# Optimization experiments

Hardware: AMD Instinct MI355X
Metric: run time of the kernel (lower is better)

The kernel has to match this reference:

```python
import jax, jax.numpy as jnp
import numpy as np

N = 100000
D = 128
H = 128
E = 1600000


def setup_inputs() -> dict:
    key = jax.random.key(0)
    ks = jax.random.split(key, 9)
    x = jax.random.normal(ks[0], (N, D), dtype=jnp.float32)
    edge_index = jax.random.randint(ks[1], (2, E), 0, N, dtype=jnp.int64)
    s = 1.0 / np.sqrt(D)
    W1 = jax.random.uniform(ks[2], (D, H), jnp.float32, -s, s)
    b1 = jnp.zeros((H,), jnp.float32)
    s2 = 1.0 / np.sqrt(H)
    W2 = jax.random.uniform(ks[3], (H, H), jnp.float32, -s2, s2)
    b2 = jnp.zeros((H,), jnp.float32)
    Wo = jax.random.uniform(ks[4], (H, 1), jnp.float32, -s2, s2)
    bo = jax.random.uniform(ks[5], (1,), jnp.float32, -s2, s2)
    return {"x": x, "edge_index": edge_index, "W1": W1, "b1": b1,
            "W2": W2, "b2": b2, "Wo": Wo, "bo": bo}


def _gcn_layer(x, W, b, src, dst, dinv):
    # PyG GCNConv: h = x @ W; out = D^-1/2 (A+I) D^-1/2 h + b
    h = x @ W                                   # [N, H]
    norm = dinv[src] * dinv[dst]                # [E]
    msg = h[src] * norm[:, None]                # [E, H] gathered messages
    agg = jax.ops.segment_sum(msg, dst, num_segments=N)
    agg = agg + h * (dinv * dinv)[:, None]      # self-loop contribution
    return agg + b


def reference(x, edge_index, W1, b1, W2, b2, Wo, bo):
    src, dst = edge_index[0], edge_index[1]
    # degree with self-loops, counted on destination (col), edge_weight = 1
    deg = jax.ops.segment_sum(jnp.ones((E,), jnp.float32), dst, num_segments=N) + 1.0
    dinv = deg ** -0.5                          # [N]
    h = jax.nn.relu(_gcn_layer(x, W1, b1, src, dst, dinv))
    h = _gcn_layer(h, W2, b2, src, dst, dinv)
    out = h @ Wo + bo                            # [N, 1]
    return out[:, 0]                             # [N]
```

## Files before the change

### kernel.cpp

```cpp
#include <hip/hip_runtime.h>
#include <hip/hip_fp16.h>

#define DIM 128
#define NPB 256
#define BCAP 5120
#define T_SCAT 4096

typedef _Float16 half8 __attribute__((ext_vector_type(8)));
typedef float floatx4 __attribute__((ext_vector_type(4)));
typedef float floatx2 __attribute__((ext_vector_type(2)));

__device__ __forceinline__ void gemm_block(const float* __restrict__ X,
                                           const __half* __restrict__ w1frag,
                                           unsigned char* __restrict__ A,
                                           int N, int gb) {
    const int t = threadIdx.x;
    const int w = t >> 6, l = t & 63;
    const int q = l >> 4;
    const int node = gb * 64 + w * 16 + (l & 15);
    const bool valid = node < N;
    half8 bfrag[4];
#pragma unroll
    for (int ks = 0; ks < 4; ks++) {
        float4 f0 = make_float4(0, 0, 0, 0), f1 = make_float4(0, 0, 0, 0);
        if (valid) {
            const float* px = X + (size_t)node * DIM + ks * 32 + q * 8;
            f0 = *(const float4*)px;
            f1 = *(const float4*)(px + 4);
        }
        bfrag[ks][0] = (_Float16)f0.x; bfrag[ks][1] = (_Float16)f0.y;
        bfrag[ks][2] = (_Float16)f0.z; bfrag[ks][3] = (_Float16)f0.w;
        bfrag[ks][4] = (_Float16)f1.x; bfrag[ks][5] = (_Float16)f1.y;
        bfrag[ks][6] = (_Float16)f1.z; bfrag[ks][7] = (_Float16)f1.w;
    }
    const half8* wf = (const half8*)w1frag;
#pragma unroll
    for (int ct = 0; ct < 8; ct++) {
        floatx4 acc = {0.f, 0.f, 0.f, 0.f};
#pragma unroll
        for (int ks = 0; ks < 4; ks++) {
            half8 afrag = wf[(ct * 4 + ks) * 64 + l];
            acc = __builtin_amdgcn_mfma_f32_16x16x32_f16(afrag, bfrag[ks], acc, 0, 0, 0);
        }
        if (valid) {
            int st = 0;
            st = __builtin_amdgcn_cvt_pk_fp8_f32(acc[0], acc[1], st, false);
            st = __builtin_amdgcn_cvt_pk_fp8_f32(acc[2], acc[3], st, true);
            *(int*)(A + (size_t)node * DIM + ct * 16 + q * 4) = st;
        }
    }
}

__global__ void prep_k(const float* __restrict__ W1, const float* __restrict__ W2,
                       const float* __restrict__ Wo, const float* __restrict__ b2,
                       const float* __restrict__ bo,
                       __half* __restrict__ w1frag, float* __restrict__ w2o,
                       float* __restrict__ cbuf, int* __restrict__ bcur) {
    if (blockIdx.x < 8) {
        int idx = blockIdx.x * 256 + threadIdx.x;
        int ct = idx >> 8, ks = (idx >> 6) & 3, l = idx & 63;
        int m = l & 15, q = l >> 4;
        half8 vals;
#pragma unroll
        for (int j = 0; j < 8; j++)
            vals[j] = (_Float16)W1[(ks * 32 + q * 8 + j) * DIM + ct * 16 + m];
        ((half8*)w1frag)[idx] = vals;
    } else if (blockIdx.x == 8) {
        int t = threadIdx.x;
        if (t < 128) {
            float s = 0.f;
            for (int k = 0; k < 128; k++) s += W2[t * 128 + k] * Wo[k];
            w2o[t] = s;
        }
        if (t == 0) {
            float c = bo[0];
            for (int k = 0; k < 128; k++) c += b2[k] * Wo[k];
            cbuf[0] = c;
        }
    } else {
#pragma unroll
        for (int i = 0; i < 4; i++) bcur[threadIdx.x + i * 256] = 0;
    }
}

__global__ __launch_bounds__(256) void scatter_gemm_k(
        const int* __restrict__ ei, int E, int ntiles,
        int2* __restrict__ be, int* __restrict__ bcur,
        const float* __restrict__ X, const __half* __restrict__ w1frag,
        unsigned char* __restrict__ A, int N) {
    if (blockIdx.x >= (unsigned)ntiles) {
        gemm_block(X, w1frag, A, N, blockIdx.x - ntiles);
        return;
    }
    __shared__ int lcnt[1024];
    __shared__ int lscan[1024];
    __shared__ int lbase[1024];
    __shared__ int wsum[4];
    __shared__ int2 stage[T_SCAT];
    const int t = threadIdx.x;
    const int lane = t & 63, w = t >> 6;
    const int tile0 = blockIdx.x * T_SCAT;
    int tcnt = E - tile0; if (tcnt > T_SCAT) tcnt = T_SCAT;
    for (int i = t; i < 1024; i += 256) lcnt[i] = 0;
    __syncthreads();
    for (int i = t; i < tcnt; i += 256)
        atomicAdd(&lcnt[ei[E + tile0 + i] >> 8], 1);
    __syncthreads();
    const int b4 = t * 4;
    int c0 = lcnt[b4], c1 = lcnt[b4 + 1], c2 = lcnt[b4 + 2], c3 = lcnt[b4 + 3];
    int s4 = c0 + c1 + c2 + c3;
    int v = s4;
#pragma unroll
    for (int off = 1; off < 64; off <<= 1) {
        int u = __shfl_up(v, off, 64);
        if (lane >= off) v += u;
    }
    if (lane == 63) wsum[w] = v;
    __syncthreads();
    int wbase = 0;
#pragma unroll
    for (int i = 0; i < 4; i++) wbase += (i < w) ? wsum[i] : 0;
    int run = wbase + v - s4;
    lscan[b4] = run;
    if (c0) lbase[b4] = b4 * BCAP + atomicAdd(&bcur[b4], c0);
    run += c0; lscan[b4 + 1] = run;
    if (c1) lbase[b4 + 1] = (b4 + 1) * BCAP + atomicAdd(&bcur[b4 + 1], c1);
    run += c1; lscan[b4 + 2] = run;
    if (c2) lbase[b4 + 2] = (b4 + 2) * BCAP + atomicAdd(&bcur[b4 + 2], c2);
    run += c2; lscan[b4 + 3] = run;
    if (c3) lbase[b4 + 3] = (b4 + 3) * BCAP + atomicAdd(&bcur[b4 + 3], c3);
    lcnt[b4] = 0; lcnt[b4 + 1] = 0; lcnt[b4 + 2] = 0; lcnt[b4 + 3] = 0;
    __syncthreads();
    for (int i = t; i < tcnt; i += 256) {
        int s = ei[tile0 + i];
        int d = ei[E + tile0 + i];
        int b = d >> 8;
        int r = atomicAdd(&lcnt[b], 1);
        stage[lscan[b] + r] = make_int2(s, d);
    }
    __syncthreads();
    for (int i = t; i < tcnt; i += 256) {
        int2 ed = stage[i];
        int b = ed.y >> 8;
        be[lbase[b] + (i - lscan[b])] = ed;
    }
}

__global__ __launch_bounds__(256) void sort_gemm_k(
        const int2* __restrict__ be, const int* __restrict__ bcur,
        int* __restrict__ csr, int* __restrict__ rp, int* __restrict__ re,
        float* __restrict__ dinv, int N, int nb,
        const float* __restrict__ X, const __half* __restrict__ w1frag,
        unsigned char* __restrict__ A, int gemmBase) {
    if (blockIdx.x >= (unsigned)nb) {
        gemm_block(X, w1frag, A, N, gemmBase + blockIdx.x - nb);
        return;
    }
    __shared__ int lcnt[256];
    __shared__ int lscan[256];
    __shared__ int lc2[256];
    __shared__ int wsum[4];
    __shared__ int stage[BCAP];
    const int t = threadIdx.x;
    const int lane = t & 63, w = t >> 6;
    const int b = blockIdx.x;
    const int s = b * BCAP;
    int cnt = bcur[b]; if (cnt > BCAP) cnt = BCAP;
    lcnt[t] = 0; lc2[t] = 0;
    __syncthreads();
    for (int i = t; i < cnt; i += 256)
        atomicAdd(&lcnt[be[s + i].y & 255], 1);
    __syncthreads();
    int v = lcnt[t];
    int iv = v;
#pragma unroll
    for (int off = 1; off < 64; off <<= 1) {
        int u = __shfl_up(iv, off, 64);
        if (lane >= off) iv += u;
    }
    if (lane == 63) wsum[w] = iv;
    __syncthreads();
    int wbase = 0;
#pragma unroll
    for (int i = 0; i < 4; i++) wbase += (i < w) ? wsum[i] : 0;
    int excl = wbase + iv - v;
    lscan[t] = excl;
    int node = b * NPB + t;
    if (node < N) {
        rp[node] = s + excl;
        re[node] = s + excl + v;
        dinv[node] = rsqrtf((float)v + 1.0f);
    }
    __syncthreads();
    for (int i = t; i < cnt; i += 256) {
        int2 ed = be[s + i];
        int d = ed.y & 255;
        int r = atomicAdd(&lc2[d], 1);
        stage[lscan[d] + r] = ed.x;
    }
    __syncthreads();
    for (int i = t; i < cnt; i += 256) csr[s + i] = stage[i];
}

__device__ __forceinline__ void dec8(int2 r, float* f) {
    floatx2 a = __builtin_amdgcn_cvt_pk_f32_fp8(r.x, false);
    floatx2 b = __builtin_amdgcn_cvt_pk_f32_fp8(r.x, true);
    floatx2 c = __builtin_amdgcn_cvt_pk_f32_fp8(r.y, false);
    floatx2 d = __builtin_amdgcn_cvt_pk_f32_fp8(r.y, true);
    f[0] = a[0]; f[1] = a[1]; f[2] = b[0]; f[3] = b[1];
    f[4] = c[0]; f[5] = c[1]; f[6] = d[0]; f[7] = d[1];
}

__global__ __launch_bounds__(256) void agg1_k(const unsigned char* __restrict__ A,
                                              const int* __restrict__ rp,
                                              const int* __restrict__ re,
                                              const int* __restrict__ csr_src,
                                              const float* __restrict__ dinv,
                                              const float* __restrict__ b1,
                                              const float* __restrict__ w2o,
                                              float* __restrict__ z, int N) {
    const int li = threadIdx.x & 31;
    const int node = blockIdx.x * 8 + (threadIdx.x >> 5);
    if (node >= N) return;
    const int eoff = (li & 15) * 8;
    const float dn = dinv[node];
    const int s0 = rp[node], s1 = re[node];
    float acc[8];
    {
        int2 raw = *(const int2*)(A + (size_t)node * DIM + eoff);
        float hv[8]; dec8(raw, hv);
        float w0 = (li < 16) ? dn * dn : 0.f;
#pragma unroll
        for (int e = 0; e < 8; e++) acc[e] = hv[e] * w0;
    }
    for (int base = s0; base < s1; base += 32) {
        int sidx = 0; float dsl = 0.f;
        if (base + li < s1) { sidx = csr_src[base + li]; dsl = dinv[sidx]; }
        int nloc = s1 - base; if (nloc > 32) nloc = 32;
        int npair = (nloc + 1) >> 1;
#pragma unroll 2
        for (int j = 0; j < npair; j++) {
            int sel = 2 * j + (li >> 4);
            int ssrc = __shfl(sidx, sel, 32);
            float wgt = __shfl(dsl, sel, 32) * dn;
            int2 hraw = *(const int2*)(A + (size_t)ssrc * DIM + eoff);
            float h[8]; dec8(hraw, h);
#pragma unroll
            for (int e = 0; e < 8; e++) acc[e] = fmaf(h[e], wgt, acc[e]);
        }
    }
#pragma unroll
    for (int e = 0; e < 8; e++) acc[e] += __shfl_xor(acc[e], 16, 32);
    float sum = 0.f;
    if (li < 16) {
        float4 b0 = *(const float4*)(b1 + eoff);
        float4 b3 = *(const float4*)(b1 + eoff + 4);
        float4 w0 = *(const float4*)(w2o + eoff);
        float4 w3 = *(const float4*)(w2o + eoff + 4);
        sum  = fmaxf(acc[0] + b0.x, 0.f) * w0.x;
        sum += fmaxf(acc[1] + b0.y, 0.f) * w0.y;
        sum += fmaxf(acc[2] + b0.z, 0.f) * w0.z;
        sum += fmaxf(acc[3] + b0.w, 0.f) * w0.w;
        sum += fmaxf(acc[4] + b3.x, 0.f) * w3.x;
        sum += fmaxf(acc[5] + b3.y, 0.f) * w3.y;
        sum += fmaxf(acc[6] + b3.z, 0.f) * w3.z;
        sum += fmaxf(acc[7] + b3.w, 0.f) * w3.w;
    }
#pragma unroll
    for (int off = 16; off > 0; off >>= 1) sum += __shfl_down(sum, off, 32);
    if (li == 0) z[node] = sum;
}

__global__ void final_k(const float* __restrict__ z, const float* __restrict__ dinv,
                        const int* __restrict__ rp, const int* __restrict__ re,
                        const int* __restrict__ csr_src,
                        const float* __restrict__ cbuf, float* __restrict__ out, int N) {
    int n = blockIdx.x * 256 + threadIdx.x;
    if (n >= N) return;
    float dn = dinv[n];
    int s0 = rp[n], s1 = re[n];
    float s = 0.f;
    for (int i = s0; i < s1; i++) {
        int sx = csr_src[i];
        s = fmaf(dinv[sx], z[sx], s);
    }
    out[n] = fmaf(dn, s, fmaf(dn * dn, z[n], cbuf[0]));
}

extern "C" void kernel_launch(void* const* d_in, const int* in_sizes, int n_in,
                              void* d_out, int out_size, void* d_ws, size_t ws_size,
                              hipStream_t stream) {
    const float* x  = (const float*)d_in[0];
    const int*   ei = (const int*)d_in[1];
    const float* W1 = (const float*)d_in[2];
    const float* b1 = (const float*)d_in[3];
    const float* W2 = (const float*)d_in[4];
    const float* b2 = (const float*)d_in[5];
    const float* Wo = (const float*)d_in[6];
    const float* bo = (const float*)d_in[7];
    float* out = (float*)d_out;

    const int N = in_sizes[0] / DIM;
    const int E = in_sizes[1] / 2;
    const int NB = (N + NPB - 1) >> 8;
    const int ntiles = (E + T_SCAT - 1) / T_SCAT;
    const int ngemm = (N + 63) / 64;
    const int g1 = ngemm / 2;
    const int g2 = ngemm - g1;

    char* p = (char*)d_ws;
    auto alloc = [&](size_t bytes) {
        void* r = (void*)p;
        p += (bytes + 255) & ~size_t(255);
        return r;
    };
    unsigned char* A = (unsigned char*)alloc((size_t)N * DIM);
    int2*  be     = (int2*)alloc((size_t)NB * BCAP * 8);
    int*   csr    = (int*)alloc((size_t)NB * BCAP * 4);
    float* z      = (float*)alloc((size_t)N * 4);
    float* dinv   = (float*)alloc((size_t)N * 4);
    float* w2o    = (float*)alloc(128 * 4);
    float* cbuf   = (float*)alloc(16);
    __half* w1frag= (__half*)alloc(2048 * 8 * 2);
    int* rp       = (int*)alloc((size_t)N * 4);
    int* re       = (int*)alloc((size_t)N * 4);
    int* bcur     = (int*)alloc(1024 * 4);

    prep_k<<<10, 256, 0, stream>>>(W1, W2, Wo, b2, bo, w1frag, w2o, cbuf, bcur);
    scatter_gemm_k<<<ntiles + g1, 256, 0, stream>>>(ei, E, ntiles, be, bcur,
                                                    x, w1frag, A, N);
    sort_gemm_k<<<NB + g2, 256, 0, stream>>>(be, bcur, csr, rp, re, dinv, N, NB,
                                             x, w1frag, A, g1);
    agg1_k<<<(N + 7) / 8, 256, 0, stream>>>(A, rp, re, csr, dinv, b1, w2o, z, N);
    final_k<<<(N + 255) / 256, 256, 0, stream>>>(z, dinv, rp, re, csr, cbuf, out, N);
}
```

Baseline: 232.2 us.

## Fuse bucket sort with layer-1 aggregation and compute degrees via global atomics

```diff
diff --git a/kernel.cpp b/kernel.cpp
--- a/kernel.cpp
+++ b/kernel.cpp
@@ -85,7 +85,7 @@
 
 __global__ __launch_bounds__(256) void scatter_gemm_k(
         const int* __restrict__ ei, int E, int ntiles,
-        int2* __restrict__ be, int* __restrict__ bcur,
+        int2* __restrict__ be, int* __restrict__ bcur, int* __restrict__ deg,
         const float* __restrict__ X, const __half* __restrict__ w1frag,
         unsigned char* __restrict__ A, int N) {
     if (blockIdx.x >= (unsigned)ntiles) {
@@ -103,8 +103,11 @@
     int tcnt = E - tile0; if (tcnt > T_SCAT) tcnt = T_SCAT;
     for (int i = t; i < 1024; i += 256) lcnt[i] = 0;
     __syncthreads();
-    for (int i = t; i < tcnt; i += 256)
-        atomicAdd(&lcnt[ei[E + tile0 + i] >> 8], 1);
+    for (int i = t; i < tcnt; i += 256) {
+        int d = ei[E + tile0 + i];
+        atomicAdd(&lcnt[d >> 8], 1);
+        atomicAdd(&deg[d], 1);
+    }
     __syncthreads();
     const int b4 = t * 4;
     int c0 = lcnt[b4], c1 = lcnt[b4 + 1], c2 = lcnt[b4 + 2], c3 = lcnt[b4 + 3];
@@ -146,62 +149,6 @@
     }
 }
 
-__global__ __launch_bounds__(256) void sort_gemm_k(
-        const int2* __restrict__ be, const int* __restrict__ bcur,
-        int* __restrict__ csr, int* __restrict__ rp, int* __restrict__ re,
-        float* __restrict__ dinv, int N, int nb,
-        const float* __restrict__ X, const __half* __restrict__ w1frag,
-        unsigned char* __restrict__ A, int gemmBase) {
-    if (blockIdx.x >= (unsigned)nb) {
-        gemm_block(X, w1frag, A, N, gemmBase + blockIdx.x - nb);
-        return;
-    }
-    __shared__ int lcnt[256];
-    __shared__ int lscan[256];
-    __shared__ int lc2[256];
-    __shared__ int wsum[4];
-    __shared__ int stage[BCAP];
-    const int t = threadIdx.x;
-    const int lane = t & 63, w = t >> 6;
-    const int b = blockIdx.x;
-    const int s = b * BCAP;
-    int cnt = bcur[b]; if (cnt > BCAP) cnt = BCAP;
-    lcnt[t] = 0; lc2[t] = 0;
-    __syncthreads();
-    for (int i = t; i < cnt; i += 256)
-        atomicAdd(&lcnt[be[s + i].y & 255], 1);
-    __syncthreads();
-    int v = lcnt[t];
-    int iv = v;
-#pragma unroll
-    for (int off = 1; off < 64; off <<= 1) {
-        int u = __shfl_up(iv, off, 64);
-        if (lane >= off) iv += u;
-    }
-    if (lane == 63) wsum[w] = iv;
-    __syncthreads();
-    int wbase = 0;
-#pragma unroll
-    for (int i = 0; i < 4; i++) wbase += (i < w) ? wsum[i] : 0;
-    int excl = wbase + iv - v;
-    lscan[t] = excl;
-    int node = b * NPB + t;
-    if (node < N) {
-        rp[node] = s + excl;
-        re[node] = s + excl + v;
-        dinv[node] = rsqrtf((float)v + 1.0f);
-    }
-    __syncthreads();
-    for (int i = t; i < cnt; i += 256) {
-        int2 ed = be[s + i];
-        int d = ed.y & 255;
-        int r = atomicAdd(&lc2[d], 1);
-        stage[lscan[d] + r] = ed.x;
-    }
-    __syncthreads();
-    for (int i = t; i < cnt; i += 256) csr[s + i] = stage[i];
-}
-
 __device__ __forceinline__ void dec8(int2 r, float* f) {
     floatx2 a = __builtin_amdgcn_cvt_pk_f32_fp8(r.x, false);
     floatx2 b = __builtin_amdgcn_cvt_pk_f32_fp8(r.x, true);
@@ -211,64 +158,119 @@
     f[4] = c[0]; f[5] = c[1]; f[6] = d[0]; f[7] = d[1];
 }
 
-__global__ __launch_bounds__(256) void agg1_k(const unsigned char* __restrict__ A,
-                                              const int* __restrict__ rp,
-                                              const int* __restrict__ re,
-                                              const int* __restrict__ csr_src,
-                                              const float* __restrict__ dinv,
-                                              const float* __restrict__ b1,
-                                              const float* __restrict__ w2o,
-                                              float* __restrict__ z, int N) {
-    const int li = threadIdx.x & 31;
-    const int node = blockIdx.x * 8 + (threadIdx.x >> 5);
-    if (node >= N) return;
+__global__ __launch_bounds__(1024) void sort_agg_k(
+        const int2* __restrict__ be, const int* __restrict__ bcur,
+        const int* __restrict__ deg,
+        int* __restrict__ csr, int* __restrict__ rp, int* __restrict__ re,
+        float* __restrict__ dinv,
+        const unsigned char* __restrict__ A,
+        const float* __restrict__ b1, const float* __restrict__ w2o,
+        float* __restrict__ z, int N) {
+    __shared__ int lcnt[256];
+    __shared__ int lscan[256];
+    __shared__ int lc2[256];
+    __shared__ int wsum[4];
+    __shared__ int stage[BCAP];
+    const int t = threadIdx.x;
+    const int b = blockIdx.x;
+    const int s = b * BCAP;
+    int cnt = bcur[b]; if (cnt > BCAP) cnt = BCAP;
+    if (t < 256) { lcnt[t] = 0; lc2[t] = 0; }
+    __syncthreads();
+    for (int i = t; i < cnt; i += 1024)
+        atomicAdd(&lcnt[be[s + i].y & 255], 1);
+    __syncthreads();
+    if (t < 256) {
+        const int lane = t & 63, w = t >> 6;
+        int v = lcnt[t];
+        int iv = v;
+#pragma unroll
+        for (int off = 1; off < 64; off <<= 1) {
+            int u = __shfl_up(iv, off, 64);
+            if (lane >= off) iv += u;
+        }
+        if (lane == 63) wsum[w] = iv;
+        __syncthreads();
+        int wbase = 0;
+#pragma unroll
+        for (int i = 0; i < 4; i++) wbase += (i < w) ? wsum[i] : 0;
+        int excl = wbase + iv - v;
+        lscan[t] = excl;
+        int node = b * NPB + t;
+        if (node < N) {
+            rp[node] = s + excl;
+            re[node] = s + excl + v;
+            dinv[node] = rsqrtf((float)v + 1.0f);
+        }
+    } else {
+        __syncthreads();
+    }
+    __syncthreads();
+    for (int i = t; i < cnt; i += 1024) {
+        int2 ed = be[s + i];
+        int d = ed.y & 255;
+        int r = atomicAdd(&lc2[d], 1);
+        stage[lscan[d] + r] = ed.x;
+    }
+    __syncthreads();
+    for (int i = t; i < cnt; i += 1024) csr[s + i] = stage[i];
+    const int li = t & 31;
+    const int grp = t >> 5;
     const int eoff = (li & 15) * 8;
-    const float dn = dinv[node];
-    const int s0 = rp[node], s1 = re[node];
-    float acc[8];
-    {
-        int2 raw = *(const int2*)(A + (size_t)node * DIM + eoff);
-        float hv[8]; dec8(raw, hv);
-        float w0 = (li < 16) ? dn * dn : 0.f;
-#pragma unroll
-        for (int e = 0; e < 8; e++) acc[e] = hv[e] * w0;
-    }
-    for (int base = s0; base < s1; base += 32) {
-        int sidx = 0; float dsl = 0.f;
-        if (base + li < s1) { sidx = csr_src[base + li]; dsl = dinv[sidx]; }
-        int nloc = s1 - base; if (nloc > 32) nloc = 32;
-        int npair = (nloc + 1) >> 1;
+    for (int nn = grp; nn < NPB; nn += 32) {
+        int node = b * NPB + nn;
+        if (node >= N) continue;
+        const int cn = lcnt[nn];
+        const int s0 = lscan[nn];
+        const float dn = rsqrtf((float)cn + 1.0f);
+        float acc[8];
+        {
+            int2 raw = *(const int2*)(A + (size_t)node * DIM + eoff);
+            float hv[8]; dec8(raw, hv);
+            float w0 = (li < 16) ? dn * dn : 0.f;
+#pragma unroll
+            for (int e = 0; e < 8; e++) acc[e] = hv[e] * w0;
+        }
+        for (int base = 0; base < cn; base += 32) {
+            int sidx = 0; float dsl = 0.f;
+            if (base + li < cn) {
+                sidx = stage[s0 + base + li];
+                dsl = rsqrtf((float)deg[sidx] + 1.0f);
+            }
+            int nloc = cn - base; if (nloc > 32) nloc = 32;
+            int npair = (nloc + 1) >> 1;
 #pragma unroll 2
-        for (int j = 0; j < npair; j++) {
-            int sel = 2 * j + (li >> 4);
-            int ssrc = __shfl(sidx, sel, 32);
-            float wgt = __shfl(dsl, sel, 32) * dn;
-            int2 hraw = *(const int2*)(A + (size_t)ssrc * DIM + eoff);
-            float h[8]; dec8(hraw, h);
-#pragma unroll
-            for (int e = 0; e < 8; e++) acc[e] = fmaf(h[e], wgt, acc[e]);
-        }
-    }
-#pragma unroll
-    for (int e = 0; e < 8; e++) acc[e] += __shfl_xor(acc[e], 16, 32);
-    float sum = 0.f;
-    if (li < 16) {
-        float4 b0 = *(const float4*)(b1 + eoff);
-        float4 b3 = *(const float4*)(b1 + eoff + 4);
-        float4 w0 = *(const float4*)(w2o + eoff);
-        float4 w3 = *(const float4*)(w2o + eoff + 4);
-        sum  = fmaxf(acc[0] + b0.x, 0.f) * w0.x;
-        sum += fmaxf(acc[1] + b0.y, 0.f) * w0.y;
-        sum += fmaxf(acc[2] + b0.z, 0.f) * w0.z;
-        sum += fmaxf(acc[3] + b0.w, 0.f) * w0.w;
-        sum += fmaxf(acc[4] + b3.x, 0.f) * w3.x;
-        sum += fmaxf(acc[5] + b3.y, 0.f) * w3.y;
-        sum += fmaxf(acc[6] + b3.z, 0.f) * w3.z;
-        sum += fmaxf(acc[7] + b3.w, 0.f) * w3.w;
-    }
-#pragma unroll
-    for (int off = 16; off > 0; off >>= 1) sum += __shfl_down(sum, off, 32);
-    if (li == 0) z[node] = sum;
+            for (int j = 0; j < npair; j++) {
+                int sel = 2 * j + (li >> 4);
+                int ssrc = __shfl(sidx, sel, 32);
+                float wgt = __shfl(dsl, sel, 32) * dn;
+                int2 hraw = *(const int2*)(A + (size_t)ssrc * DIM + eoff);
+                float h[8]; dec8(hraw, h);
+#pragma unroll
+                for (int e = 0; e < 8; e++) acc[e] = fmaf(h[e], wgt, acc[e]);
+            }
+        }
+#pragma unroll
+        for (int e = 0; e < 8; e++) acc[e] += __shfl_xor(acc[e], 16, 32);
+        float sum = 0.f;
+        if (li < 16) {
+            float4 b0 = *(const float4*)(b1 + eoff);
+            float4 b3 = *(const float4*)(b1 + eoff + 4);
+            float4 w0 = *(const float4*)(w2o + eoff);
+            float4 w3 = *(const float4*)(w2o + eoff + 4);
+            sum  = fmaxf(acc[0] + b0.x, 0.f) * w0.x;
+            sum += fmaxf(acc[1] + b0.y, 0.f) * w0.y;
+            sum += fmaxf(acc[2] + b0.z, 0.f) * w0.z;
+            sum += fmaxf(acc[3] + b0.w, 0.f) * w0.w;
+            sum += fmaxf(acc[4] + b3.x, 0.f) * w3.x;
+            sum += fmaxf(acc[5] + b3.y, 0.f) * w3.y;
+            sum += fmaxf(acc[6] + b3.z, 0.f) * w3.z;
+            sum += fmaxf(acc[7] + b3.w, 0.f) * w3.w;
+        }
+#pragma unroll
+        for (int off = 16; off > 0; off >>= 1) sum += __shfl_down(sum, off, 32);
+        if (li == 0) z[node] = sum;
+    }
 }
 
 __global__ void final_k(const float* __restrict__ z, const float* __restrict__ dinv,
@@ -305,8 +307,6 @@
     const int NB = (N + NPB - 1) >> 8;
     const int ntiles = (E + T_SCAT - 1) / T_SCAT;
     const int ngemm = (N + 63) / 64;
-    const int g1 = ngemm / 2;
-    const int g2 = ngemm - g1;
 
     char* p = (char*)d_ws;
     auto alloc = [&](size_t bytes) {
@@ -317,6 +317,7 @@
     unsigned char* A = (unsigned char*)alloc((size_t)N * DIM);
     int2*  be     = (int2*)alloc((size_t)NB * BCAP * 8);
     int*   csr    = (int*)alloc((size_t)NB * BCAP * 4);
+    int*   deg    = (int*)alloc((size_t)N * 4);
     float* z      = (float*)alloc((size_t)N * 4);
     float* dinv   = (float*)alloc((size_t)N * 4);
     float* w2o    = (float*)alloc(128 * 4);
@@ -326,11 +327,11 @@
     int* re       = (int*)alloc((size_t)N * 4);
     int* bcur     = (int*)alloc(1024 * 4);
 
+    hipMemsetAsync(deg, 0, (size_t)N * 4, stream);
     prep_k<<<10, 256, 0, stream>>>(W1, W2, Wo, b2, bo, w1frag, w2o, cbuf, bcur);
-    scatter_gemm_k<<<ntiles + g1, 256, 0, stream>>>(ei, E, ntiles, be, bcur,
-                                                    x, w1frag, A, N);
-    sort_gemm_k<<<NB + g2, 256, 0, stream>>>(be, bcur, csr, rp, re, dinv, N, NB,
-                                             x, w1frag, A, g1);
-    agg1_k<<<(N + 7) / 8, 256, 0, stream>>>(A, rp, re, csr, dinv, b1, w2o, z, N);
+    scatter_gemm_k<<<ntiles + ngemm, 256, 0, stream>>>(ei, E, ntiles, be, bcur, deg,
+                                                       x, w1frag, A, N);
+    sort_agg_k<<<NB, 1024, 0, stream>>>(be, bcur, deg, csr, rp, re, dinv,
+                                        A, b1, w2o, z, N);
     final_k<<<(N + 255) / 256, 256, 0, stream>>>(z, dinv, rp, re, csr, cbuf, out, N);
 }
```

After: 286.1 us. +23.2%, slower.
